# Performance work log

Measured on AMD Instinct MI355X. Metric: run time of the kernel, lower is better.

## Reference

```python
import jax, jax.numpy as jnp
import numpy as np

H = 768
NH = 12
HD = H // NH  # 64


def setup_inputs() -> dict:
    key = jax.random.key(0)
    ks = jax.random.split(key, 12)
    B, SQ, SK = 8, 1024, 1024
    s = 1.0 / np.sqrt(H)
    return {
        "hidden_states": jax.random.normal(ks[0], (B, SQ, H), jnp.float32),
        "condition_embeddings": jax.random.normal(ks[1], (B, SK, H), jnp.float32),
        "condition_mask": jnp.ones((B, SK), jnp.float32),
        "Wq": jax.random.normal(ks[2], (H, H), jnp.float32) * s,
        "bq": jnp.zeros((H,), jnp.float32),
        "Wk": jax.random.normal(ks[3], (H, H), jnp.float32) * s,
        "bk": jnp.zeros((H,), jnp.float32),
        "Wv": jax.random.normal(ks[4], (H, H), jnp.float32) * s,
        "bv": jnp.zeros((H,), jnp.float32),
        "Wo": jax.random.normal(ks[5], (H, H), jnp.float32) * s,
        "bo": jnp.zeros((H,), jnp.float32),
        "ln_g": jnp.ones((H,), jnp.float32),
        "ln_b": jnp.zeros((H,), jnp.float32),
    }


def _heads(x):
    # [B, S, H] -> [B, NH, S, HD]
    B, S, _ = x.shape
    return x.reshape(B, S, NH, HD).transpose(0, 2, 1, 3)


def reference(hidden_states, condition_embeddings, condition_mask,
              Wq, bq, Wk, bk, Wv, bv, Wo, bo, ln_g, ln_b):
    q = _heads(hidden_states @ Wq.T + bq)            # [B,NH,SQ,HD]
    k = _heads(condition_embeddings @ Wk.T + bk)     # [B,NH,SK,HD]
    v = _heads(condition_embeddings @ Wv.T + bv)     # [B,NH,SK,HD]

    scores = jnp.einsum("bhqd,bhkd->bhqk", q, k) / np.sqrt(HD)
    ext_mask = (1.0 - condition_mask)[:, None, None, :] * -10000.0
    scores = scores + ext_mask
    probs = jax.nn.softmax(scores, axis=-1)          # dropout = identity (eval)

    ctx = jnp.einsum("bhqk,bhkd->bhqd", probs, v)    # [B,NH,SQ,HD]
    B, _, SQ, _ = ctx.shape
    ctx = ctx.transpose(0, 2, 1, 3).reshape(B, SQ, H)

    out = ctx @ Wo.T + bo
    x = hidden_states + out
    mu = jnp.mean(x, axis=-1, keepdims=True)
    var = jnp.var(x, axis=-1, keepdims=True)
    return (x - mu) / jnp.sqrt(var + 1e-5) * ln_g + ln_b
```

## Files before the change

### kernel.cpp

```cpp
#include <hip/hip_runtime.h>
#include <stdint.h>

#define B_ 8
#define S_ 1024
#define H_ 768
#define NH_ 12
#define HD_ 64
#define M_ (B_*S_)

typedef __attribute__((ext_vector_type(8))) short short8;
typedef __attribute__((ext_vector_type(8))) ushort ushort8;
typedef __attribute__((ext_vector_type(4))) float floatx4;

#define MFMA16(a,b,c) __builtin_amdgcn_mfma_f32_16x16x32_bf16((a),(b),(c),0,0,0)

__device__ __forceinline__ ushort f2bf(float x){
    union { float f; unsigned u; } v; v.f = x;
    unsigned r = (v.u + 0x7fffu + ((v.u >> 16) & 1u)) >> 16;
    return (ushort)r;
}

__device__ __forceinline__ void async16(const ushort* g, ushort* l){
    __builtin_amdgcn_global_load_lds(
        (const __attribute__((address_space(1))) unsigned int*)g,
        (__attribute__((address_space(3))) unsigned int*)l, 16, 0, 0);
}

__global__ __launch_bounds__(256, 8) void cvt_all(
    const float* __restrict__ hs, const float* __restrict__ ce,
    const float* __restrict__ wq, const float* __restrict__ wk,
    const float* __restrict__ wv, const float* __restrict__ wo,
    ushort* __restrict__ hsb, ushort* __restrict__ ceb,
    ushort* __restrict__ wqb, ushort* __restrict__ wkb,
    ushort* __restrict__ wvb, ushort* __restrict__ wob)
{
    const int NA = M_*H_/8;
    const int NW = H_*H_/8;
    int i = blockIdx.x*256 + threadIdx.x;
    if (i >= 2*NA + 4*NW) return;
    const float* s; ushort* d; int off;
    if (i < NA)            { s = hs; d = hsb; off = i; }
    else if (i < 2*NA)     { s = ce; d = ceb; off = i - NA; }
    else {
        int j = i - 2*NA;
        int wsel = j / NW;
        off = j - wsel*NW;
        s = (wsel==0) ? wq : (wsel==1) ? wk : (wsel==2) ? wv : wo;
        d = (wsel==0) ? wqb : (wsel==1) ? wkb : (wsel==2) ? wvb : wob;
    }
    float4 f0 = ((const float4*)s)[2*off];
    float4 f1 = ((const float4*)s)[2*off + 1];
    ushort8 u;
    u[0] = f2bf(f0.x); u[1] = f2bf(f0.y); u[2] = f2bf(f0.z); u[3] = f2bf(f0.w);
    u[4] = f2bf(f1.x); u[5] = f2bf(f1.y); u[6] = f2bf(f1.z); u[7] = f2bf(f1.w);
    ((ushort8*)d)[off] = u;
}

template<int BN, int MODE>
__device__ __forceinline__ void gemm_body(
    ushort* __restrict__ smem,
    const ushort* __restrict__ A, const ushort* __restrict__ Bw,
    const float* __restrict__ bias, ushort* __restrict__ obf,
    float* __restrict__ of32, const float* __restrict__ resid,
    int bx, int by)
{
    constexpr int NT = BN/32;
    ushort* lA = smem;
    ushort* lB = smem + 8192;
    const int K = H_;
    int tid  = threadIdx.x;
    int lane = tid & 63, wave = tid >> 6;
    int m0 = bx * 128, n0 = by * BN;
    int wm = (wave >> 1) * 64, wn = (wave & 1) * (BN/2);
    int fr = lane & 15, quad = lane >> 4, quad4 = quad*4;

    floatx4 acc[4][NT];
    #pragma unroll
    for (int mt=0;mt<4;mt++)
        #pragma unroll
        for (int nt=0;nt<NT;nt++)
            acc[mt][nt] = (floatx4){0.f,0.f,0.f,0.f};

    int row0 = tid >> 3;
    int csw  = ((tid & 7) ^ (row0 & 7)) * 8;
    const ushort* Ap[4]; const ushort* Bp[NT];
    ushort* ldA_[4]; ushort* ldB_[NT];
    #pragma unroll
    for (int j=0;j<4;j++){
        int row = row0 + 32*j;
        Ap[j] = A + (size_t)(m0 + row) * K + csw;
        ldA_[j] = lA + (tid + 256*j)*8;
    }
    #pragma unroll
    for (int j=0;j<NT;j++){
        int row = row0 + 32*j;
        Bp[j] = Bw + (size_t)(n0 + row) * K + csw;
        ldB_[j] = lB + (tid + 256*j)*8;
    }

    for (int k0 = 0; k0 < K; k0 += 64){
        #pragma unroll
        for (int j=0;j<4;j++) async16(Ap[j] + k0, ldA_[j]);
        #pragma unroll
        for (int j=0;j<NT;j++) async16(Bp[j] + k0, ldB_[j]);
        __syncthreads();
        #pragma unroll
        for (int kk=0; kk<2; kk++){
            short8 af[4], bfr[NT];
            #pragma unroll
            for (int t=0;t<4;t++){
                int ra = wm + t*16 + fr;
                af[t]  = *(const short8*)&lA[ra*64 + (((kk*4+quad) ^ (ra&7))<<3)];
            }
            #pragma unroll
            for (int t=0;t<NT;t++){
                int rb = wn + t*16 + fr;
                bfr[t] = *(const short8*)&lB[rb*64 + (((kk*4+quad) ^ (rb&7))<<3)];
            }
            #pragma unroll
            for (int mt=0;mt<4;mt++)
                #pragma unroll
                for (int nt=0;nt<NT;nt++)
                    acc[mt][nt] = MFMA16(af[mt], bfr[nt], acc[mt][nt]);
        }
        __syncthreads();
    }

    float bv_[NT];
    #pragma unroll
    for (int nt=0;nt<NT;nt++) bv_[nt] = bias[n0 + wn + nt*16 + fr];

    if constexpr (MODE == 0){
        #pragma unroll
        for (int mt=0;mt<4;mt++){
            int rb = m0 + wm + mt*16 + quad4;
            #pragma unroll
            for (int nt=0;nt<NT;nt++){
                int col = n0 + wn + nt*16 + fr;
                #pragma unroll
                for (int r=0;r<4;r++)
                    obf[(size_t)(rb + r)*H_ + col] = f2bf(acc[mt][nt][r] + bv_[nt]);
            }
        }
    } else {
        #pragma unroll
        for (int mt=0;mt<4;mt++){
            int rb = m0 + wm + mt*16 + quad4;
            #pragma unroll
            for (int nt=0;nt<NT;nt++){
                int col = n0 + wn + nt*16 + fr;
                #pragma unroll
                for (int r=0;r<4;r++){
                    size_t idx = (size_t)(rb + r)*H_ + col;
                    of32[idx] = acc[mt][nt][r] + bv_[nt] + resid[idx];
                }
            }
        }
    }
}

__device__ __forceinline__ void gemm_kv_body(
    ushort* __restrict__ smem,
    const ushort* __restrict__ A,
    const ushort* __restrict__ Bk, const ushort* __restrict__ Bv,
    const float* __restrict__ biask, const float* __restrict__ biasv,
    ushort* __restrict__ Kb, ushort* __restrict__ Vtb,
    int bx, int by)
{
    ushort* lA  = smem;
    ushort* lBK = smem + 8192;
    ushort* lBV = smem + 14336;
    const int K = H_;
    int tid  = threadIdx.x;
    int lane = tid & 63, wave = tid >> 6;
    int m0 = bx * 128, n0 = by * 96;
    int wm = (wave >> 1) * 64, wn = (wave & 1) * 48;
    int fr = lane & 15, quad = lane >> 4, quad4 = quad*4;

    floatx4 aK[4][3], aV[4][3];
    #pragma unroll
    for (int mt=0;mt<4;mt++)
        #pragma unroll
        for (int nt=0;nt<3;nt++){
            aK[mt][nt] = (floatx4){0.f,0.f,0.f,0.f};
            aV[mt][nt] = (floatx4){0.f,0.f,0.f,0.f};
        }

    int row0 = tid >> 3;
    int csw  = ((tid & 7) ^ (row0 & 7)) * 8;
    const ushort* Ap[4]; const ushort* Kp[3]; const ushort* Vp[3];
    ushort* ldA_[4]; ushort* ldK_[3]; ushort* ldV_[3];
    #pragma unroll
    for (int j=0;j<4;j++){
        int row = row0 + 32*j;
        Ap[j] = A + (size_t)(m0 + row) * K + csw;
        ldA_[j] = lA + (tid + 256*j)*8;
    }
    #pragma unroll
    for (int j=0;j<3;j++){
        int row = row0 + 32*j;
        Kp[j] = Bk + (size_t)(n0 + row) * K + csw;
        Vp[j] = Bv + (size_t)(n0 + row) * K + csw;
        ldK_[j] = lBK + (tid + 256*j)*8;
        ldV_[j] = lBV + (tid + 256*j)*8;
    }

    for (int k0 = 0; k0 < K; k0 += 64){
        #pragma unroll
        for (int j=0;j<4;j++) async16(Ap[j] + k0, ldA_[j]);
        #pragma unroll
        for (int j=0;j<3;j++) async16(Kp[j] + k0, ldK_[j]);
        #pragma unroll
        for (int j=0;j<3;j++) async16(Vp[j] + k0, ldV_[j]);
        __syncthreads();
        #pragma unroll
        for (int kk=0; kk<2; kk++){
            short8 af[4], bk_[3], bv2_[3];
            #pragma unroll
            for (int t=0;t<4;t++){
                int ra = wm + t*16 + fr;
                af[t] = *(const short8*)&lA[ra*64 + (((kk*4+quad) ^ (ra&7))<<3)];
            }
            #pragma unroll
            for (int t=0;t<3;t++){
                int rb = wn + t*16 + fr;
                int off = (((kk*4+quad) ^ (rb&7))<<3);
                bk_[t]  = *(const short8*)&lBK[rb*64 + off];
                bv2_[t] = *(const short8*)&lBV[rb*64 + off];
            }
            #pragma unroll
            for (int mt=0;mt<4;mt++)
                #pragma unroll
                for (int nt=0;nt<3;nt++){
                    aK[mt][nt] = MFMA16(af[mt], bk_[nt],  aK[mt][nt]);
                    aV[mt][nt] = MFMA16(af[mt], bv2_[nt], aV[mt][nt]);
                }
        }
        __syncthreads();
    }

    float bk4[3], bv4[3];
    #pragma unroll
    for (int nt=0;nt<3;nt++){
        bk4[nt] = biask[n0 + wn + nt*16 + fr];
        bv4[nt] = biasv[n0 + wn + nt*16 + fr];
    }

    #pragma unroll
    for (int mt=0;mt<4;mt++){
        int rb = m0 + wm + mt*16 + quad4;
        #pragma unroll
        for (int nt=0;nt<3;nt++){
            int col = n0 + wn + nt*16 + fr;
            #pragma unroll
            for (int r=0;r<4;r++)
                Kb[(size_t)(rb + r)*H_ + col] = f2bf(aK[mt][nt][r] + bk4[nt]);
        }
    }

    int bb = m0 >> 10, q0 = m0 & 1023;
    #pragma unroll
    for (int mt=0;mt<4;mt++){
        int ql = wm + mt*16 + quad4;
        #pragma unroll
        for (int nt=0;nt<3;nt++){
            int dl = wn + nt*16 + fr;
            ushort4 u;
            u.x = f2bf(aV[mt][nt][0] + bv4[nt]);
            u.y = f2bf(aV[mt][nt][1] + bv4[nt]);
            u.z = f2bf(aV[mt][nt][2] + bv4[nt]);
            u.w = f2bf(aV[mt][nt][3] + bv4[nt]);
            *(ushort4*)&smem[dl*136 + ql] = u;
        }
    }
    __syncthreads();
    #pragma unroll
    for (int jj=0;jj<6;jj++){
        int mI = tid + 256*jj;
        int d  = mI >> 4;
        int qc = (mI & 15) * 8;
        short8 v = *(const short8*)&smem[d*136 + qc];
        int gcol = by*96 + d;
        int h = gcol >> 6, dd = gcol & 63;
        *(short8*)&Vtb[((size_t)((bb*NH_ + h)*HD_ + dd))*S_ + q0 + qc] = v;
    }
}

__global__ __launch_bounds__(256, 3) void gemm_qkv(
    const ushort* __restrict__ hsb, const ushort* __restrict__ ceb,
    const ushort* __restrict__ wqb, const ushort* __restrict__ wkb,
    const ushort* __restrict__ wvb,
    const float* __restrict__ bq, const float* __restrict__ bk,
    const float* __restrict__ bv,
    ushort* __restrict__ Qb, ushort* __restrict__ Kb, ushort* __restrict__ Vtb)
{
    __shared__ ushort smem[20480];
    int by = blockIdx.y;
    if (by < 4)
        gemm_body<192,0>(smem, hsb, wqb, bq, Qb, nullptr, nullptr,
                         blockIdx.x, by);
    else
        gemm_kv_body(smem, ceb, wkb, wvb, bk, bv, Kb, Vtb,
                     blockIdx.x, by - 4);
}

__global__ __launch_bounds__(256, 3) void gemm_o(
    const ushort* __restrict__ ctxb, const ushort* __restrict__ wob,
    const float* __restrict__ bo, const float* __restrict__ hs,
    float* __restrict__ proj)
{
    __shared__ ushort smem[8192 + 96*64];
    gemm_body<96,2>(smem, ctxb, wob, bo, nullptr, proj, hs,
                    blockIdx.x, blockIdx.y);
}

__global__ __launch_bounds__(256, 3) void attn(
    const ushort* __restrict__ Q, const ushort* __restrict__ Kc,
    const ushort* __restrict__ Vt, const float* __restrict__ mask,
    ushort* __restrict__ ctx)
{
    __shared__ ushort lK[64*64];
    __shared__ ushort lV[64*64];
    __shared__ ushort lP[4][32*72];
    __shared__ float  lmask[S_];
    __shared__ float  linv[4][32];

    const float SC = 0.125f * 1.44269504f;

    int bid = blockIdx.x;
    int qt = bid & 7;
    int h  = (bid >> 3) % NH_;
    int b  = bid / (8*NH_);

    int tid  = threadIdx.x;
    int lane = tid & 63, w = tid >> 6;
    int fr = lane & 15, quad = lane >> 4;
    int quad4 = quad*4, sw = fr & 7;

    for (int i = tid; i < S_; i += 256)
        lmask[i] = (1.0f - mask[b*S_ + i]) * -14426.95f;

    short8 qf[2][2];
    #pragma unroll
    for (int nq=0;nq<2;nq++){
        const ushort* Qp = Q + (size_t)(b*S_ + qt*128 + w*32 + nq*16 + fr)*H_ + h*HD_ + quad*8;
        qf[nq][0] = *(const short8*)(Qp);
        qf[nq][1] = *(const short8*)(Qp + 32);
    }

    floatx4 O[2][4];
    #pragma unroll
    for (int mt=0;mt<2;mt++)
        #pragma unroll
        for (int nt=0;nt<4;nt++)
            O[mt][nt] = (floatx4){0.f,0.f,0.f,0.f};
    float rs0 = 0.f, rs1 = 0.f;

    int n0 = tid,       r0 = n0 >> 3, c0 = (n0 & 7) ^ (r0 & 7);
    int n1 = 256 + tid, r1 = n1 >> 3, c1 = (n1 & 7) ^ (r1 & 7);
    const ushort* pK0 = Kc + (size_t)(b*S_ + r0)*H_ + h*HD_ + c0*8;
    const ushort* pK1 = Kc + (size_t)(b*S_ + r1)*H_ + h*HD_ + c1*8;
    const ushort* pV0 = Vt + ((size_t)(b*NH_ + h)*HD_ + r0)*S_ + c0*8;
    const ushort* pV1 = Vt + ((size_t)(b*NH_ + h)*HD_ + r1)*S_ + c1*8;
    ushort* dK0 = &lK[n0*8]; ushort* dK1 = &lK[n1*8];
    ushort* dV0 = &lV[n0*8]; ushort* dV1 = &lV[n1*8];

    ushort* lPw = &lP[w][0];

    for (int kt = 0; kt < 16; kt++){
        __syncthreads();
        async16(pK0, dK0); async16(pK1, dK1);
        async16(pV0, dV0); async16(pV1, dV1);
        pK0 += (size_t)64*H_; pK1 += (size_t)64*H_;
        pV0 += 64; pV1 += 64;
        __syncthreads();

        float4 mk4[4];
        #pragma unroll
        for (int mk=0;mk<4;mk++)
            mk4[mk] = *(const float4*)&lmask[kt*64 + mk*16 + quad4];

        short8 kf[4][2];
        #pragma unroll
        for (int mk=0;mk<4;mk++){
            int row = mk*16 + fr;
            kf[mk][0] = *(const short8*)&lK[row*64 + ((quad     ^ sw)<<3)];
            kf[mk][1] = *(const short8*)&lK[row*64 + (((4+quad) ^ sw)<<3)];
        }
        __builtin_amdgcn_s_setprio(1);
        floatx4 st[2][4];
        #pragma unroll
        for (int nq=0;nq<2;nq++)
            #pragma unroll
            for (int mk=0;mk<4;mk++){
                floatx4 a = (floatx4){0.f,0.f,0.f,0.f};
                a = MFMA16(kf[mk][0], qf[nq][0], a);
                a = MFMA16(kf[mk][1], qf[nq][1], a);
                st[nq][mk] = a;
            }
        __builtin_amdgcn_s_setprio(0);

        #pragma unroll
        for (int nq=0;nq<2;nq++){
            #pragma unroll
            for (int mk=0;mk<4;mk++){
                floatx4 s = st[nq][mk];
                #pragma unroll
                for (int r=0;r<4;r++)
                    s[r] = __builtin_amdgcn_exp2f(s[r]*SC + mk4[mk][r]);
                if (nq == 0) rs0 += (s[0]+s[1]) + (s[2]+s[3]);
                else         rs1 += (s[0]+s[1]) + (s[2]+s[3]);
                unsigned lo = __builtin_amdgcn_perm(__float_as_uint(s[1]), __float_as_uint(s[0]), 0x07060302u);
                unsigned hi = __builtin_amdgcn_perm(__float_as_uint(s[3]), __float_as_uint(s[2]), 0x07060302u);
                uint2 pk; pk.x = lo; pk.y = hi;
                *(uint2*)&lPw[(nq*16 + fr)*72 + mk*16 + quad4] = pk;
            }
        }

        short8 vf[4][2];
        #pragma unroll
        for (int nt=0;nt<4;nt++){
            int row = nt*16 + fr;
            vf[nt][0] = *(const short8*)&lV[row*64 + ((quad     ^ sw)<<3)];
            vf[nt][1] = *(const short8*)&lV[row*64 + (((4+quad) ^ sw)<<3)];
        }
        short8 pf[2][2];
        #pragma unroll
        for (int mt=0;mt<2;mt++){
            pf[mt][0] = *(const short8*)&lPw[(mt*16+fr)*72 + quad*8];
            pf[mt][1] = *(const short8*)&lPw[(mt*16+fr)*72 + 32 + quad*8];
        }
        __builtin_amdgcn_s_setprio(1);
        #pragma unroll
        for (int mt=0;mt<2;mt++)
            #pragma unroll
            for (int nt=0;nt<4;nt++){
                O[mt][nt] = MFMA16(pf[mt][0], vf[nt][0], O[mt][nt]);
                O[mt][nt] = MFMA16(pf[mt][1], vf[nt][1], O[mt][nt]);
            }
        __builtin_amdgcn_s_setprio(0);
    }

    rs0 += __shfl_xor(rs0, 16); rs0 += __shfl_xor(rs0, 32);
    rs1 += __shfl_xor(rs1, 16); rs1 += __shfl_xor(rs1, 32);
    if (lane < 16){
        linv[w][fr]      = 1.0f / rs0;
        linv[w][16 + fr] = 1.0f / rs1;
    }
    int tokbase = b*S_ + qt*128 + w*32;
    #pragma unroll
    for (int mt=0;mt<2;mt++){
        float4 iv = *(const float4*)&linv[w][mt*16 + quad4];
        #pragma unroll
        for (int nt=0;nt<4;nt++)
            #pragma unroll
            for (int r=0;r<4;r++){
                int tok = tokbase + mt*16 + quad4 + r;
                ctx[(size_t)tok*H_ + h*HD_ + nt*16 + fr] = f2bf(O[mt][nt][r] * (&iv.x)[r]);
            }
    }
}

__global__ __launch_bounds__(192, 4) void resid_ln(
    const float* __restrict__ x,
    const float* __restrict__ g, const float* __restrict__ be,
    float* __restrict__ out)
{
    int row = blockIdx.x;
    int tid = threadIdx.x;
    float4 v = ((const float4*)(x + (size_t)row*H_))[tid];
    float s  = (v.x + v.y) + (v.z + v.w);
    float s2 = (v.x*v.x + v.y*v.y) + (v.z*v.z + v.w*v.w);
    #pragma unroll
    for (int off=1; off<64; off<<=1){
        s  += __shfl_xor(s,  off);
        s2 += __shfl_xor(s2, off);
    }
    __shared__ float rs[3], rs2[3];
    if ((tid & 63) == 0){ rs[tid>>6] = s; rs2[tid>>6] = s2; }
    __syncthreads();
    s  = rs[0]+rs[1]+rs[2];
    s2 = rs2[0]+rs2[1]+rs2[2];
    float mu  = s * (1.f/H_);
    float var = s2*(1.f/H_) - mu*mu;
    float rinv = rsqrtf(var + 1e-5f);
    float4 gg = ((const float4*)g)[tid];
    float4 bb = ((const float4*)be)[tid];
    float4 o;
    o.x = (v.x-mu)*rinv*gg.x + bb.x;
    o.y = (v.y-mu)*rinv*gg.y + bb.y;
    o.z = (v.z-mu)*rinv*gg.z + bb.z;
    o.w = (v.w-mu)*rinv*gg.w + bb.w;
    ((float4*)(out + (size_t)row*H_))[tid] = o;
}

extern "C" void kernel_launch(void* const* d_in, const int* in_sizes, int n_in,
                              void* d_out, int out_size, void* d_ws, size_t ws_size,
                              hipStream_t stream)
{
    (void)in_sizes; (void)n_in; (void)out_size; (void)ws_size;
    const float* hs   = (const float*)d_in[0];
    const float* ce   = (const float*)d_in[1];
    const float* mask = (const float*)d_in[2];
    const float* Wq   = (const float*)d_in[3];
    const float* bq   = (const float*)d_in[4];
    const float* Wk   = (const float*)d_in[5];
    const float* bk   = (const float*)d_in[6];
    const float* Wv   = (const float*)d_in[7];
    const float* bv   = (const float*)d_in[8];
    const float* Wo   = (const float*)d_in[9];
    const float* bo   = (const float*)d_in[10];
    const float* lg   = (const float*)d_in[11];
    const float* lb   = (const float*)d_in[12];
    float* out = (float*)d_out;

    char* ws = (char*)d_ws;
    const size_t SZ_ACT = (size_t)M_*H_*2;
    const size_t SZ_W   = (size_t)H_*H_*2;
    ushort* hsb  = (ushort*)(ws);
    ushort* ceb  = (ushort*)(ws + SZ_ACT);
    ushort* wqb  = (ushort*)(ws + 2*SZ_ACT);
    ushort* wkb  = (ushort*)(ws + 2*SZ_ACT + 1*SZ_W);
    ushort* wvb  = (ushort*)(ws + 2*SZ_ACT + 2*SZ_W);
    ushort* wob  = (ushort*)(ws + 2*SZ_ACT + 3*SZ_W);
    ushort* Qb   = (ushort*)(ws + 2*SZ_ACT + 4*SZ_W);
    ushort* Kb   = (ushort*)(ws + 3*SZ_ACT + 4*SZ_W);
    ushort* Vtb  = (ushort*)(ws + 4*SZ_ACT + 4*SZ_W);
    ushort* ctxb = (ushort*)(ws + 5*SZ_ACT + 4*SZ_W);
    float*  proj = (float*)(ws);

    int ncvt = 2*(M_*H_/8) + 4*(H_*H_/8);
    cvt_all<<<dim3((ncvt+255)/256), dim3(256), 0, stream>>>(
        hs, ce, Wq, Wk, Wv, Wo, hsb, ceb, wqb, wkb, wvb, wob);

    gemm_qkv<<<dim3(M_/128, 12), dim3(256), 0, stream>>>(
        hsb, ceb, wqb, wkb, wvb, bq, bk, bv, Qb, Kb, Vtb);

    attn<<<dim3(B_*NH_*8), dim3(256), 0, stream>>>(Qb, Kb, Vtb, mask, ctxb);

    gemm_o<<<dim3(M_/128, H_/96), dim3(256), 0, stream>>>(ctxb, wob, bo, hs, proj);

    resid_ln<<<dim3(M_), dim3(192), 0, stream>>>(proj, lg, lb, out);
}
```

Before: 216.2 us.

## Double-buffer K/V tiles in attention and swizzle the P buffer

The attention kernel now keeps two LDS buffers for K and V. The next tile's async global-to-LDS copy is issued before computing on the current tile, and the loop drops from two barriers per iteration to one. The P staging buffer loses its padding (stride 72 to 64) and uses an XOR swizzle to avoid bank conflicts. The separate linv array is folded into the P buffer. LDS per block grows, which could limit occupancy at three blocks per CU, and the overlap depends on how the compiler places waits on the async loads.

New measurement: 218.9 us. About the same (+1.3%).

```diff
diff --git a/kernel.cpp b/kernel.cpp
--- a/kernel.cpp
+++ b/kernel.cpp
@@ -319,11 +319,10 @@
     const ushort* __restrict__ Vt, const float* __restrict__ mask,
     ushort* __restrict__ ctx)
 {
-    __shared__ ushort lK[64*64];
-    __shared__ ushort lV[64*64];
-    __shared__ ushort lP[4][32*72];
+    __shared__ ushort lK[2][64*64];
+    __shared__ ushort lV[2][64*64];
+    __shared__ ushort lP[4][32*64];
     __shared__ float  lmask[S_];
-    __shared__ float  linv[4][32];
 
     const float SC = 0.125f * 1.44269504f;
 
@@ -336,25 +335,6 @@
     int lane = tid & 63, w = tid >> 6;
     int fr = lane & 15, quad = lane >> 4;
     int quad4 = quad*4, sw = fr & 7;
-
-    for (int i = tid; i < S_; i += 256)
-        lmask[i] = (1.0f - mask[b*S_ + i]) * -14426.95f;
-
-    short8 qf[2][2];
-    #pragma unroll
-    for (int nq=0;nq<2;nq++){
-        const ushort* Qp = Q + (size_t)(b*S_ + qt*128 + w*32 + nq*16 + fr)*H_ + h*HD_ + quad*8;
-        qf[nq][0] = *(const short8*)(Qp);
-        qf[nq][1] = *(const short8*)(Qp + 32);
-    }
-
-    floatx4 O[2][4];
-    #pragma unroll
-    for (int mt=0;mt<2;mt++)
-        #pragma unroll
-        for (int nt=0;nt<4;nt++)
-            O[mt][nt] = (floatx4){0.f,0.f,0.f,0.f};
-    float rs0 = 0.f, rs1 = 0.f;
 
     int n0 = tid,       r0 = n0 >> 3, c0 = (n0 & 7) ^ (r0 & 7);
     int n1 = 256 + tid, r1 = n1 >> 3, c1 = (n1 & 7) ^ (r1 & 7);
@@ -362,18 +342,46 @@
     const ushort* pK1 = Kc + (size_t)(b*S_ + r1)*H_ + h*HD_ + c1*8;
     const ushort* pV0 = Vt + ((size_t)(b*NH_ + h)*HD_ + r0)*S_ + c0*8;
     const ushort* pV1 = Vt + ((size_t)(b*NH_ + h)*HD_ + r1)*S_ + c1*8;
-    ushort* dK0 = &lK[n0*8]; ushort* dK1 = &lK[n1*8];
-    ushort* dV0 = &lV[n0*8]; ushort* dV1 = &lV[n1*8];
+
+    async16(pK0, &lK[0][n0*8]); async16(pK1, &lK[0][n1*8]);
+    async16(pV0, &lV[0][n0*8]); async16(pV1, &lV[0][n1*8]);
+    pK0 += (size_t)64*H_; pK1 += (size_t)64*H_;
+    pV0 += 64; pV1 += 64;
+
+    for (int i = tid; i < S_; i += 256)
+        lmask[i] = (1.0f - mask[b*S_ + i]) * -14426.95f;
+
+    short8 qf[2][2];
+    #pragma unroll
+    for (int nq=0;nq<2;nq++){
+        const ushort* Qp = Q + (size_t)(b*S_ + qt*128 + w*32 + nq*16 + fr)*H_ + h*HD_ + quad*8;
+        qf[nq][0] = *(const short8*)(Qp);
+        qf[nq][1] = *(const short8*)(Qp + 32);
+    }
+
+    floatx4 O[2][4];
+    #pragma unroll
+    for (int mt=0;mt<2;mt++)
+        #pragma unroll
+        for (int nt=0;nt<4;nt++)
+            O[mt][nt] = (floatx4){0.f,0.f,0.f,0.f};
+    float rs0 = 0.f, rs1 = 0.f;
 
     ushort* lPw = &lP[w][0];
 
+    __syncthreads();
+
     for (int kt = 0; kt < 16; kt++){
-        __syncthreads();
-        async16(pK0, dK0); async16(pK1, dK1);
-        async16(pV0, dV0); async16(pV1, dV1);
-        pK0 += (size_t)64*H_; pK1 += (size_t)64*H_;
-        pV0 += 64; pV1 += 64;
-        __syncthreads();
+        int cur = kt & 1;
+        if (kt < 15){
+            int nxt = cur ^ 1;
+            async16(pK0, &lK[nxt][n0*8]); async16(pK1, &lK[nxt][n1*8]);
+            async16(pV0, &lV[nxt][n0*8]); async16(pV1, &lV[nxt][n1*8]);
+            pK0 += (size_t)64*H_; pK1 += (size_t)64*H_;
+            pV0 += 64; pV1 += 64;
+        }
+        const ushort* Kl = lK[cur];
+        const ushort* Vl = lV[cur];
 
         float4 mk4[4];
         #pragma unroll
@@ -384,8 +392,8 @@
         #pragma unroll
         for (int mk=0;mk<4;mk++){
             int row = mk*16 + fr;
-            kf[mk][0] = *(const short8*)&lK[row*64 + ((quad     ^ sw)<<3)];
-            kf[mk][1] = *(const short8*)&lK[row*64 + (((4+quad) ^ sw)<<3)];
+            kf[mk][0] = *(const short8*)&Kl[row*64 + ((quad     ^ sw)<<3)];
+            kf[mk][1] = *(const short8*)&Kl[row*64 + (((4+quad) ^ sw)<<3)];
         }
         __builtin_amdgcn_s_setprio(1);
         floatx4 st[2][4];
@@ -413,7 +421,7 @@
                 unsigned lo = __builtin_amdgcn_perm(__float_as_uint(s[1]), __float_as_uint(s[0]), 0x07060302u);
                 unsigned hi = __builtin_amdgcn_perm(__float_as_uint(s[3]), __float_as_uint(s[2]), 0x07060302u);
                 uint2 pk; pk.x = lo; pk.y = hi;
-                *(uint2*)&lPw[(nq*16 + fr)*72 + mk*16 + quad4] = pk;
+                *(uint2*)&lPw[(nq*16 + fr)*64 + (((2*mk + (quad>>1)) ^ sw)<<3) + (quad&1)*4] = pk;
             }
         }
 
@@ -421,14 +429,14 @@
         #pragma unroll
         for (int nt=0;nt<4;nt++){
             int row = nt*16 + fr;
-            vf[nt][0] = *(const short8*)&lV[row*64 + ((quad     ^ sw)<<3)];
-            vf[nt][1] = *(const short8*)&lV[row*64 + (((4+quad) ^ sw)<<3)];
+            vf[nt][0] = *(const short8*)&Vl[row*64 + ((quad     ^ sw)<<3)];
+            vf[nt][1] = *(const short8*)&Vl[row*64 + (((4+quad) ^ sw)<<3)];
         }
         short8 pf[2][2];
         #pragma unroll
         for (int mt=0;mt<2;mt++){
-            pf[mt][0] = *(const short8*)&lPw[(mt*16+fr)*72 + quad*8];
-            pf[mt][1] = *(const short8*)&lPw[(mt*16+fr)*72 + 32 + quad*8];
+            pf[mt][0] = *(const short8*)&lPw[(mt*16+fr)*64 + ((quad     ^ sw)<<3)];
+            pf[mt][1] = *(const short8*)&lPw[(mt*16+fr)*64 + (((4+quad) ^ sw)<<3)];
         }
         __builtin_amdgcn_s_setprio(1);
         #pragma unroll
@@ -439,18 +447,21 @@
                 O[mt][nt] = MFMA16(pf[mt][1], vf[nt][1], O[mt][nt]);
             }
         __builtin_amdgcn_s_setprio(0);
+
+        __syncthreads();
     }
 
     rs0 += __shfl_xor(rs0, 16); rs0 += __shfl_xor(rs0, 32);
     rs1 += __shfl_xor(rs1, 16); rs1 += __shfl_xor(rs1, 32);
+    float* linvw = (float*)&lP[w][0];
     if (lane < 16){
-        linv[w][fr]      = 1.0f / rs0;
-        linv[w][16 + fr] = 1.0f / rs1;
+        linvw[fr]      = 1.0f / rs0;
+        linvw[16 + fr] = 1.0f / rs1;
     }
     int tokbase = b*S_ + qt*128 + w*32;
     #pragma unroll
     for (int mt=0;mt<2;mt++){
-        float4 iv = *(const float4*)&linv[w][mt*16 + quad4];
+        float4 iv = *(const float4*)&linvw[mt*16 + quad4];
         #pragma unroll
         for (int nt=0;nt<4;nt++)
             #pragma unroll
```
